# Optimization experiments

Measured on AMD Instinct MI355X. Metric: run time of the kernel, lower is better.

The kernel has to match this reference:

```python
import jax, jax.numpy as jnp
import numpy as np

B, N, D = 8, 4096, 3

def setup_inputs() -> dict:
    key = jax.random.key(0)
    kx, ky = jax.random.split(key)
    x = jax.random.normal(kx, (B, N, D), dtype=jnp.float32)
    y = jax.random.normal(ky, (B, N, D), dtype=jnp.float32)
    return {"x": x, "y": y}

def _nn_diff(A, B_):
    # brute-force NN: squared distances [N, M] via ||a||^2 + ||b||^2 - 2 a.b
    a2 = jnp.sum(A * A, axis=-1)[:, None]
    b2 = jnp.sum(B_ * B_, axis=-1)[None, :]
    d2 = a2 + b2 - 2.0 * (A @ B_.T)
    idx = jnp.argmin(d2, axis=1)            # closest point in B_ for each point in A
    return A - B_[idx]                      # [N, D] signed residuals

def _sigma_pair(S1, S2):
    d12 = _nn_diff(S1, S2)                  # S1 -> S2 residuals
    d21 = _nn_diff(S2, S1)                  # S2 -> S1 residuals
    # torch.std over the whole [N, D] tensor with Bessel's correction (ddof=1)
    std1 = jnp.std(d12, ddof=1)
    std2 = jnp.std(d21, ddof=1)
    return jnp.maximum(std1, std2)

def reference(x, y):
    per_batch = jax.vmap(_sigma_pair)(x, y)  # [B]
    return per_batch.mean()
```

## Files before the change

### kernel.cpp

```cpp
#include <hip/hip_runtime.h>
#include <math.h>

#define NPTS 4096
#define BLK 256
#define NUNITS 16
#define CHUNKS 16
#define CSZ 256
#define TILES 8
#define QGRP 256
#define QGRPS 16
#define GRID1 (NUNITS * QGRPS * CHUNKS)
#define GRID2 (NUNITS * QGRPS)
#define CNT 12288.0f
#define KEY_BYTES ((size_t)NUNITS * CHUNKS * NPTS * 4)

typedef _Float16 half8 __attribute__((ext_vector_type(8)));
typedef float f32x16 __attribute__((ext_vector_type(16)));

__device__ __forceinline__ unsigned umin2(unsigned a, unsigned b) { return a < b ? a : b; }
__device__ __forceinline__ float fmin3(float a, float b, float c) {
  return fminf(fminf(a, b), c);
}

__device__ __forceinline__ float tilemin16(const f32x16 d) {
  const float a0 = fmin3(d[0],  d[1],  d[2]);
  const float a1 = fmin3(d[3],  d[4],  d[5]);
  const float a2 = fmin3(d[6],  d[7],  d[8]);
  const float a3 = fmin3(d[9],  d[10], d[11]);
  const float a4 = fmin3(d[12], d[13], d[14]);
  return fminf(fmin3(a0, a1, a2), fmin3(a3, a4, d[15]));
}

__global__ __launch_bounds__(BLK, 4) void keys_kernel(
    const float* __restrict__ x, const float* __restrict__ y,
    unsigned* __restrict__ keys) {
  __shared__ half8 Ap[2 * CSZ];
  __shared__ half8 Bq[2 * QGRP];

  const int bid   = blockIdx.x;
  const int unit  = bid >> 8;
  const int qg    = (bid >> 4) & 15;
  const int chunk = bid & 15;
  const int b = unit >> 1, dir = unit & 1;
  const float* __restrict__ Q = (dir ? y : x) + (size_t)b * NPTS * 3;
  const float* __restrict__ T = (dir ? x : y) + (size_t)b * NPTS * 3;

  const int tid = threadIdx.x;
  const _Float16 one  = (_Float16)1.0f;
  const _Float16 zero = (_Float16)0.0f;
  const _Float16 n2   = (_Float16)(-2.0f);

  {
    const int tg = chunk * CSZ + tid;
    const float bx = T[3 * tg], by = T[3 * tg + 1], bz = T[3 * tg + 2];
    const float b2 = fmaf(bx, bx, fmaf(by, by, bz * bz));
    const _Float16 bh0 = (_Float16)bx, bh1 = (_Float16)by, bh2 = (_Float16)bz;
    const _Float16 bl0 = (_Float16)(bx - (float)bh0);
    const _Float16 bl1 = (_Float16)(by - (float)bh1);
    const _Float16 bl2 = (_Float16)(bz - (float)bh2);
    const _Float16 s2h = (_Float16)b2;
    const _Float16 s2l = (_Float16)(b2 - (float)s2h);
    half8 lo, hi;
    lo[0] = bh0; lo[1] = bh1; lo[2] = bh2; lo[3] = bl0;
    lo[4] = bl1; lo[5] = bl2; lo[6] = bh0; lo[7] = bh1;
    hi[0] = bh2; hi[1] = s2h; hi[2] = s2l; hi[3] = one;
    hi[4] = one; hi[5] = zero; hi[6] = zero; hi[7] = zero;
    Ap[tid]       = lo;
    Ap[CSZ + tid] = hi;
  }
  {
    const int qq = qg * QGRP + tid;
    const float ax = Q[3 * qq], ay = Q[3 * qq + 1], az = Q[3 * qq + 2];
    const float a2 = fmaf(ax, ax, fmaf(ay, ay, az * az));
    const _Float16 ah0 = (_Float16)ax, ah1 = (_Float16)ay, ah2 = (_Float16)az;
    const _Float16 al0 = (_Float16)(ax - (float)ah0);
    const _Float16 al1 = (_Float16)(ay - (float)ah1);
    const _Float16 al2 = (_Float16)(az - (float)ah2);
    const _Float16 a2h = (_Float16)a2;
    const _Float16 a2l = (_Float16)(a2 - (float)a2h);
    half8 lo, hi;
    lo[0] = n2 * ah0; lo[1] = n2 * ah1; lo[2] = n2 * ah2; lo[3] = n2 * ah0;
    lo[4] = n2 * ah1; lo[5] = n2 * ah2; lo[6] = n2 * al0; lo[7] = n2 * al1;
    hi[0] = n2 * al2; hi[1] = one; hi[2] = one; hi[3] = a2h;
    hi[4] = a2l; hi[5] = zero; hi[6] = zero; hi[7] = zero;
    Bq[tid]        = lo;
    Bq[QGRP + tid] = hi;
  }
  __syncthreads();

  const int lane = tid & 63, w = tid >> 6, ln = lane & 31, hi5 = lane >> 5;
  const half8 bf0 = Bq[hi5 * QGRP + w * 64 + ln];
  const half8 bf1 = Bq[hi5 * QGRP + w * 64 + 32 + ln];

  f32x16 Z;
  #pragma unroll
  for (int r = 0; r < 16; ++r) Z[r] = 0.0f;

  unsigned kacc0 = 0xFFFFFFFFu, kacc1 = 0xFFFFFFFFu;
  const unsigned pbase = (unsigned)(chunk * TILES);

  #pragma unroll
  for (int t = 0; t < TILES; ++t) {
    const half8 af = Ap[hi5 * CSZ + t * 32 + ln];
    const f32x16 d0 = __builtin_amdgcn_mfma_f32_32x32x16_f16(af, bf0, Z, 0, 0, 0);
    const f32x16 d1 = __builtin_amdgcn_mfma_f32_32x32x16_f16(af, bf1, Z, 0, 0, 0);
    const unsigned pay = pbase + (unsigned)t;
    const float m0 = tilemin16(d0);
    const float m1 = tilemin16(d1);
    kacc0 = umin2(kacc0, (__float_as_uint(m0) & 0xFFFFF000u) | pay);
    kacc1 = umin2(kacc1, (__float_as_uint(m1) & 0xFFFFF000u) | pay);
  }

  kacc0 = umin2(kacc0, (unsigned)__shfl_xor((int)kacc0, 32));
  kacc1 = umin2(kacc1, (unsigned)__shfl_xor((int)kacc1, 32));

  if (lane < 32) {
    const unsigned kb = (unsigned)((unit * CHUNKS + chunk) << 12);
    const unsigned q0 = (unsigned)(qg * QGRP + w * 64 + ln);
    keys[kb | q0]        = kacc0;
    keys[kb | (q0 + 32)] = kacc1;
  }
}

__global__ __launch_bounds__(BLK) void resolve_kernel(
    const float* __restrict__ x, const float* __restrict__ y,
    const unsigned* __restrict__ keys, float2* __restrict__ partials) {
  __shared__ float wS[4], wSS[4];

  const int bid  = blockIdx.x;
  const int unit = bid >> 4;
  const int b = unit >> 1, dir = unit & 1;
  const float* __restrict__ Q = (dir ? y : x) + (size_t)b * NPTS * 3;
  const float* __restrict__ T = (dir ? x : y) + (size_t)b * NPTS * 3;
  const int q = ((bid & 15) << 8) + (int)threadIdx.x;

  unsigned bk = 0xFFFFFFFFu;
  #pragma unroll
  for (int c = 0; c < CHUNKS; ++c) {
    bk = umin2(bk, keys[((unsigned)(unit * CHUNKS + c) << 12) | (unsigned)q]);
  }
  const int tbase = (int)(bk & 4095u) * 32;

  const float qx = Q[3 * q], qy = Q[3 * q + 1], qz = Q[3 * q + 2];
  unsigned best = 0xFFFFFFFFu;
  #pragma unroll 8
  for (int i = 0; i < 32; ++i) {
    const int j = tbase + i;
    const float dx = qx - T[3 * j];
    const float dy = qy - T[3 * j + 1];
    const float dz = qz - T[3 * j + 2];
    const float d2 = fmaf(dx, dx, fmaf(dy, dy, dz * dz));
    best = umin2(best, (__float_as_uint(d2) & 0xFFFFFFE0u) | (unsigned)i);
  }
  const int j = tbase + (int)(best & 31u);

  const float rx = qx - T[3 * j];
  const float ry = qy - T[3 * j + 1];
  const float rz = qz - T[3 * j + 2];
  float s  = rx + ry + rz;
  float ss = fmaf(rx, rx, fmaf(ry, ry, rz * rz));

  #pragma unroll
  for (int off = 32; off > 0; off >>= 1) {
    s  += __shfl_down(s, off);
    ss += __shfl_down(ss, off);
  }
  const int wid = threadIdx.x >> 6;
  if ((threadIdx.x & 63) == 0) { wS[wid] = s; wSS[wid] = ss; }
  __syncthreads();
  if (threadIdx.x == 0) {
    partials[bid] = make_float2(wS[0] + wS[1] + wS[2] + wS[3],
                                wSS[0] + wSS[1] + wSS[2] + wSS[3]);
  }
}

__global__ __launch_bounds__(256) void finalize_kernel(
    const float2* __restrict__ partials, float* __restrict__ out) {
  __shared__ float2 sh[GRID2];
  __shared__ float sig[NUNITS];

  sh[threadIdx.x] = partials[threadIdx.x];
  __syncthreads();

  if (threadIdx.x < NUNITS) {
    float S = 0.f, SS = 0.f;
    #pragma unroll
    for (int i = 0; i < QGRPS; ++i) {
      S  += sh[threadIdx.x * QGRPS + i].x;
      SS += sh[threadIdx.x * QGRPS + i].y;
    }
    const float var = (SS - S * S / CNT) / (CNT - 1.0f);
    sig[threadIdx.x] = sqrtf(fmaxf(var, 0.0f));
  }
  __syncthreads();

  if (threadIdx.x == 0) {
    float acc = 0.f;
    #pragma unroll
    for (int b = 0; b < 8; ++b) acc += fmaxf(sig[2 * b], sig[2 * b + 1]);
    out[0] = acc * 0.125f;
  }
}

extern "C" void kernel_launch(void* const* d_in, const int* in_sizes, int n_in,
                              void* d_out, int out_size, void* d_ws, size_t ws_size,
                              hipStream_t stream) {
  const float* x = (const float*)d_in[0];
  const float* y = (const float*)d_in[1];
  float* out = (float*)d_out;

  unsigned* keys   = (unsigned*)d_ws;
  float2*  partials = (float2*)((char*)d_ws + KEY_BYTES);

  hipLaunchKernelGGL(keys_kernel, dim3(GRID1), dim3(BLK), 0, stream, x, y, keys);
  hipLaunchKernelGGL(resolve_kernel, dim3(GRID2), dim3(BLK), 0, stream,
                     x, y, keys, partials);
  hipLaunchKernelGGL(finalize_kernel, dim3(1), dim3(256), 0, stream, partials, out);
}
```

Baseline: 25.62 us.

## Halve key chunks and fuse finalize into resolve via last-block ticket

Doubles the target chunk size per block (CHUNKS 16→8, TILES 8→16), halving the keys-kernel grid and the number of partial keys that resolve must min-reduce. It also folds the finalize kernel into the resolve kernel: each block publishes its partial sums atomically and takes a ticket, and the last block to arrive computes the final sigma mean. This removes one kernel launch and its dependency gap, at the cost of less parallelism in the keys kernel, more LDS per block, and a grid-wide atomic counter that keys_kernel resets.

```diff
diff --git a/kernel.cpp b/kernel.cpp
--- a/kernel.cpp
+++ b/kernel.cpp
@@ -4,9 +4,9 @@
 #define NPTS 4096
 #define BLK 256
 #define NUNITS 16
-#define CHUNKS 16
-#define CSZ 256
-#define TILES 8
+#define CHUNKS 8
+#define CSZ 512
+#define TILES 16
 #define QGRP 256
 #define QGRPS 16
 #define GRID1 (NUNITS * QGRPS * CHUNKS)
@@ -33,25 +33,29 @@
 
 __global__ __launch_bounds__(BLK, 4) void keys_kernel(
     const float* __restrict__ x, const float* __restrict__ y,
-    unsigned* __restrict__ keys) {
+    unsigned* __restrict__ keys, unsigned* __restrict__ ticket) {
   __shared__ half8 Ap[2 * CSZ];
   __shared__ half8 Bq[2 * QGRP];
 
   const int bid   = blockIdx.x;
-  const int unit  = bid >> 8;
-  const int qg    = (bid >> 4) & 15;
-  const int chunk = bid & 15;
+  const int unit  = bid >> 7;
+  const int qg    = (bid >> 3) & 15;
+  const int chunk = bid & 7;
   const int b = unit >> 1, dir = unit & 1;
   const float* __restrict__ Q = (dir ? y : x) + (size_t)b * NPTS * 3;
   const float* __restrict__ T = (dir ? x : y) + (size_t)b * NPTS * 3;
 
   const int tid = threadIdx.x;
+  if (bid == 0 && tid == 0) *ticket = 0;
+
   const _Float16 one  = (_Float16)1.0f;
   const _Float16 zero = (_Float16)0.0f;
   const _Float16 n2   = (_Float16)(-2.0f);
 
-  {
-    const int tg = chunk * CSZ + tid;
+  #pragma unroll
+  for (int k = 0; k < 2; ++k) {
+    const int i  = tid + k * BLK;
+    const int tg = chunk * CSZ + i;
     const float bx = T[3 * tg], by = T[3 * tg + 1], bz = T[3 * tg + 2];
     const float b2 = fmaf(bx, bx, fmaf(by, by, bz * bz));
     const _Float16 bh0 = (_Float16)bx, bh1 = (_Float16)by, bh2 = (_Float16)bz;
@@ -65,8 +69,8 @@
     lo[4] = bl1; lo[5] = bl2; lo[6] = bh0; lo[7] = bh1;
     hi[0] = bh2; hi[1] = s2h; hi[2] = s2l; hi[3] = one;
     hi[4] = one; hi[5] = zero; hi[6] = zero; hi[7] = zero;
-    Ap[tid]       = lo;
-    Ap[CSZ + tid] = hi;
+    Ap[i]       = lo;
+    Ap[CSZ + i] = hi;
   }
   {
     const int qq = qg * QGRP + tid;
@@ -122,17 +126,23 @@
   }
 }
 
-__global__ __launch_bounds__(BLK) void resolve_kernel(
+__global__ __launch_bounds__(BLK) void resolve_finalize_kernel(
     const float* __restrict__ x, const float* __restrict__ y,
-    const unsigned* __restrict__ keys, float2* __restrict__ partials) {
+    const unsigned* __restrict__ keys,
+    unsigned long long* __restrict__ partials,
+    unsigned* __restrict__ ticket, float* __restrict__ out) {
   __shared__ float wS[4], wSS[4];
+  __shared__ unsigned lastsh;
+  __shared__ float2 sh[GRID2];
+  __shared__ float sig[NUNITS];
 
   const int bid  = blockIdx.x;
   const int unit = bid >> 4;
   const int b = unit >> 1, dir = unit & 1;
   const float* __restrict__ Q = (dir ? y : x) + (size_t)b * NPTS * 3;
   const float* __restrict__ T = (dir ? x : y) + (size_t)b * NPTS * 3;
-  const int q = ((bid & 15) << 8) + (int)threadIdx.x;
+  const int tid = threadIdx.x;
+  const int q = ((bid & 15) << 8) + tid;
 
   unsigned bk = 0xFFFFFFFFu;
   #pragma unroll
@@ -165,39 +175,46 @@
     s  += __shfl_down(s, off);
     ss += __shfl_down(ss, off);
   }
-  const int wid = threadIdx.x >> 6;
-  if ((threadIdx.x & 63) == 0) { wS[wid] = s; wSS[wid] = ss; }
-  __syncthreads();
-  if (threadIdx.x == 0) {
-    partials[bid] = make_float2(wS[0] + wS[1] + wS[2] + wS[3],
-                                wSS[0] + wSS[1] + wSS[2] + wSS[3]);
-  }
-}
-
-__global__ __launch_bounds__(256) void finalize_kernel(
-    const float2* __restrict__ partials, float* __restrict__ out) {
-  __shared__ float2 sh[GRID2];
-  __shared__ float sig[NUNITS];
-
-  sh[threadIdx.x] = partials[threadIdx.x];
-  __syncthreads();
-
-  if (threadIdx.x < NUNITS) {
+  const int wid = tid >> 6;
+  if ((tid & 63) == 0) { wS[wid] = s; wSS[wid] = ss; }
+  __syncthreads();
+
+  if (tid == 0) {
+    const float S  = wS[0]  + wS[1]  + wS[2]  + wS[3];
+    const float SS = wSS[0] + wSS[1] + wSS[2] + wSS[3];
+    const unsigned long long pv =
+        ((unsigned long long)__float_as_uint(SS) << 32) | __float_as_uint(S);
+    atomicExch(&partials[bid], pv);
+    __threadfence();
+    lastsh = atomicAdd(ticket, 1u);
+  }
+  __syncthreads();
+  if (lastsh != GRID2 - 1) return;
+
+  __threadfence();
+  {
+    const unsigned long long pv = atomicAdd(&partials[tid], 0ULL);
+    sh[tid] = make_float2(__uint_as_float((unsigned)(pv & 0xFFFFFFFFull)),
+                          __uint_as_float((unsigned)(pv >> 32)));
+  }
+  __syncthreads();
+
+  if (tid < NUNITS) {
     float S = 0.f, SS = 0.f;
     #pragma unroll
     for (int i = 0; i < QGRPS; ++i) {
-      S  += sh[threadIdx.x * QGRPS + i].x;
-      SS += sh[threadIdx.x * QGRPS + i].y;
+      S  += sh[tid * QGRPS + i].x;
+      SS += sh[tid * QGRPS + i].y;
     }
     const float var = (SS - S * S / CNT) / (CNT - 1.0f);
-    sig[threadIdx.x] = sqrtf(fmaxf(var, 0.0f));
-  }
-  __syncthreads();
-
-  if (threadIdx.x == 0) {
+    sig[tid] = sqrtf(fmaxf(var, 0.0f));
+  }
+  __syncthreads();
+
+  if (tid == 0) {
     float acc = 0.f;
     #pragma unroll
-    for (int b = 0; b < 8; ++b) acc += fmaxf(sig[2 * b], sig[2 * b + 1]);
+    for (int b2 = 0; b2 < 8; ++b2) acc += fmaxf(sig[2 * b2], sig[2 * b2 + 1]);
     out[0] = acc * 0.125f;
   }
 }
@@ -209,11 +226,14 @@
   const float* y = (const float*)d_in[1];
   float* out = (float*)d_out;
 
-  unsigned* keys   = (unsigned*)d_ws;
-  float2*  partials = (float2*)((char*)d_ws + KEY_BYTES);
-
-  hipLaunchKernelGGL(keys_kernel, dim3(GRID1), dim3(BLK), 0, stream, x, y, keys);
-  hipLaunchKernelGGL(resolve_kernel, dim3(GRID2), dim3(BLK), 0, stream,
-                     x, y, keys, partials);
-  hipLaunchKernelGGL(finalize_kernel, dim3(1), dim3(256), 0, stream, partials, out);
-}
+  unsigned* keys = (unsigned*)d_ws;
+  unsigned long long* partials =
+      (unsigned long long*)((char*)d_ws + KEY_BYTES);
+  unsigned* ticket =
+      (unsigned*)((char*)d_ws + KEY_BYTES + GRID2 * sizeof(unsigned long long));
+
+  hipLaunchKernelGGL(keys_kernel, dim3(GRID1), dim3(BLK), 0, stream,
+                     x, y, keys, ticket);
+  hipLaunchKernelGGL(resolve_finalize_kernel, dim3(GRID2), dim3(BLK), 0, stream,
+                     x, y, keys, partials, ticket, out);
+}
```

Result: slower. 27.89 us (+8.8%).

## Fuse key scan and resolve into one full-scan kernel per query group

Applied to the files above, without the earlier changes.

The separate keys and resolve kernels are replaced by a single kernel. Each block stages all 4096 target points into LDS in two 2048-point phases, runs the MFMA distance scan for 128 queries, then refines the winning 32-point tile and reduces the residual sums in place. This removes the global key workspace write and re-read and one kernel launch. In exchange, each target point is converted to fp16 hi/lo form twice as often in total, each block uses much more LDS, and the grid shrinks to 512 blocks with lower occupancy. Half of each wave sits idle during the refinement step.

```diff
diff --git a/kernel.cpp b/kernel.cpp
--- a/kernel.cpp
+++ b/kernel.cpp
@@ -4,15 +4,11 @@
 #define NPTS 4096
 #define BLK 256
 #define NUNITS 16
-#define CHUNKS 16
-#define CSZ 256
-#define TILES 8
-#define QGRP 256
-#define QGRPS 16
-#define GRID1 (NUNITS * QGRPS * CHUNKS)
-#define GRID2 (NUNITS * QGRPS)
+#define QGRP 128
+#define QGRPS 32
+#define GRID1 (NUNITS * QGRPS)
+#define PHT 2048
 #define CNT 12288.0f
-#define KEY_BYTES ((size_t)NUNITS * CHUNKS * NPTS * 4)
 
 typedef _Float16 half8 __attribute__((ext_vector_type(8)));
 typedef float f32x16 __attribute__((ext_vector_type(16)));
@@ -31,16 +27,15 @@
   return fminf(fmin3(a0, a1, a2), fmin3(a3, a4, d[15]));
 }
 
-__global__ __launch_bounds__(BLK, 4) void keys_kernel(
+__global__ __launch_bounds__(BLK, 2) void fullscan_kernel(
     const float* __restrict__ x, const float* __restrict__ y,
-    unsigned* __restrict__ keys) {
-  __shared__ half8 Ap[2 * CSZ];
+    float2* __restrict__ partials) {
+  __shared__ half8 Ap[2 * PHT];
   __shared__ half8 Bq[2 * QGRP];
+  __shared__ float wS[4], wSS[4];
 
-  const int bid   = blockIdx.x;
-  const int unit  = bid >> 8;
-  const int qg    = (bid >> 4) & 15;
-  const int chunk = bid & 15;
+  const int bid  = blockIdx.x;
+  const int unit = bid >> 5, qg = bid & 31;
   const int b = unit >> 1, dir = unit & 1;
   const float* __restrict__ Q = (dir ? y : x) + (size_t)b * NPTS * 3;
   const float* __restrict__ T = (dir ? x : y) + (size_t)b * NPTS * 3;
@@ -50,25 +45,7 @@
   const _Float16 zero = (_Float16)0.0f;
   const _Float16 n2   = (_Float16)(-2.0f);
 
-  {
-    const int tg = chunk * CSZ + tid;
-    const float bx = T[3 * tg], by = T[3 * tg + 1], bz = T[3 * tg + 2];
-    const float b2 = fmaf(bx, bx, fmaf(by, by, bz * bz));
-    const _Float16 bh0 = (_Float16)bx, bh1 = (_Float16)by, bh2 = (_Float16)bz;
-    const _Float16 bl0 = (_Float16)(bx - (float)bh0);
-    const _Float16 bl1 = (_Float16)(by - (float)bh1);
-    const _Float16 bl2 = (_Float16)(bz - (float)bh2);
-    const _Float16 s2h = (_Float16)b2;
-    const _Float16 s2l = (_Float16)(b2 - (float)s2h);
-    half8 lo, hi;
-    lo[0] = bh0; lo[1] = bh1; lo[2] = bh2; lo[3] = bl0;
-    lo[4] = bl1; lo[5] = bl2; lo[6] = bh0; lo[7] = bh1;
-    hi[0] = bh2; hi[1] = s2h; hi[2] = s2l; hi[3] = one;
-    hi[4] = one; hi[5] = zero; hi[6] = zero; hi[7] = zero;
-    Ap[tid]       = lo;
-    Ap[CSZ + tid] = hi;
-  }
-  {
+  if (tid < QGRP) {
     const int qq = qg * QGRP + tid;
     const float ax = Q[3 * qq], ay = Q[3 * qq + 1], az = Q[3 * qq + 2];
     const float a2 = fmaf(ax, ax, fmaf(ay, ay, az * az));
@@ -86,100 +63,95 @@
     Bq[tid]        = lo;
     Bq[QGRP + tid] = hi;
   }
-  __syncthreads();
 
   const int lane = tid & 63, w = tid >> 6, ln = lane & 31, hi5 = lane >> 5;
-  const half8 bf0 = Bq[hi5 * QGRP + w * 64 + ln];
-  const half8 bf1 = Bq[hi5 * QGRP + w * 64 + 32 + ln];
-
+  unsigned kacc0 = 0xFFFFFFFFu, kacc1 = 0xFFFFFFFFu;
   f32x16 Z;
   #pragma unroll
   for (int r = 0; r < 16; ++r) Z[r] = 0.0f;
 
-  unsigned kacc0 = 0xFFFFFFFFu, kacc1 = 0xFFFFFFFFu;
-  const unsigned pbase = (unsigned)(chunk * TILES);
+  half8 bf;
+  for (int c = 0; c < 2; ++c) {
+    __syncthreads();
+    #pragma unroll
+    for (int k = 0; k < 8; ++k) {
+      const int i  = tid + k * BLK;
+      const int tg = c * PHT + i;
+      const float bx = T[3 * tg], by = T[3 * tg + 1], bz = T[3 * tg + 2];
+      const float b2 = fmaf(bx, bx, fmaf(by, by, bz * bz));
+      const _Float16 bh0 = (_Float16)bx, bh1 = (_Float16)by, bh2 = (_Float16)bz;
+      const _Float16 bl0 = (_Float16)(bx - (float)bh0);
+      const _Float16 bl1 = (_Float16)(by - (float)bh1);
+      const _Float16 bl2 = (_Float16)(bz - (float)bh2);
+      const _Float16 s2h = (_Float16)b2;
+      const _Float16 s2l = (_Float16)(b2 - (float)s2h);
+      half8 lo, hi;
+      lo[0] = bh0; lo[1] = bh1; lo[2] = bh2; lo[3] = bl0;
+      lo[4] = bl1; lo[5] = bl2; lo[6] = bh0; lo[7] = bh1;
+      hi[0] = bh2; hi[1] = s2h; hi[2] = s2l; hi[3] = one;
+      hi[4] = one; hi[5] = zero; hi[6] = zero; hi[7] = zero;
+      Ap[i]       = lo;
+      Ap[PHT + i] = hi;
+    }
+    __syncthreads();
+    if (c == 0) bf = Bq[hi5 * QGRP + w * 32 + ln];
 
-  #pragma unroll
-  for (int t = 0; t < TILES; ++t) {
-    const half8 af = Ap[hi5 * CSZ + t * 32 + ln];
-    const f32x16 d0 = __builtin_amdgcn_mfma_f32_32x32x16_f16(af, bf0, Z, 0, 0, 0);
-    const f32x16 d1 = __builtin_amdgcn_mfma_f32_32x32x16_f16(af, bf1, Z, 0, 0, 0);
-    const unsigned pay = pbase + (unsigned)t;
-    const float m0 = tilemin16(d0);
-    const float m1 = tilemin16(d1);
-    kacc0 = umin2(kacc0, (__float_as_uint(m0) & 0xFFFFF000u) | pay);
-    kacc1 = umin2(kacc1, (__float_as_uint(m1) & 0xFFFFF000u) | pay);
+    const unsigned cb = (unsigned)(c * (PHT / 32));
+    #pragma unroll 4
+    for (int t = 0; t < PHT / 32; ++t) {
+      const half8 af = Ap[hi5 * PHT + t * 32 + ln];
+      const f32x16 d = __builtin_amdgcn_mfma_f32_32x32x16_f16(af, bf, Z, 0, 0, 0);
+      const unsigned key = (__float_as_uint(tilemin16(d)) & 0xFFFFF000u) | (cb + (unsigned)t);
+      if (t & 1) kacc1 = umin2(kacc1, key);
+      else       kacc0 = umin2(kacc0, key);
+    }
   }
+  unsigned kacc = umin2(kacc0, kacc1);
+  kacc = umin2(kacc, (unsigned)__shfl_xor((int)kacc, 32));
 
-  kacc0 = umin2(kacc0, (unsigned)__shfl_xor((int)kacc0, 32));
-  kacc1 = umin2(kacc1, (unsigned)__shfl_xor((int)kacc1, 32));
-
+  float s = 0.f, ss = 0.f;
   if (lane < 32) {
-    const unsigned kb = (unsigned)((unit * CHUNKS + chunk) << 12);
-    const unsigned q0 = (unsigned)(qg * QGRP + w * 64 + ln);
-    keys[kb | q0]        = kacc0;
-    keys[kb | (q0 + 32)] = kacc1;
+    const int q = qg * QGRP + w * 32 + ln;
+    const int tbase = (int)(kacc & 4095u) * 32;
+    const float qx = Q[3 * q], qy = Q[3 * q + 1], qz = Q[3 * q + 2];
+    unsigned best = 0xFFFFFFFFu;
+    #pragma unroll 8
+    for (int i = 0; i < 32; ++i) {
+      const int j = tbase + i;
+      const float dx = qx - T[3 * j];
+      const float dy = qy - T[3 * j + 1];
+      const float dz = qz - T[3 * j + 2];
+      const float d2 = fmaf(dx, dx, fmaf(dy, dy, dz * dz));
+      best = umin2(best, (__float_as_uint(d2) & 0xFFFFFFE0u) | (unsigned)i);
+    }
+    const int j = tbase + (int)(best & 31u);
+    const float rx = qx - T[3 * j];
+    const float ry = qy - T[3 * j + 1];
+    const float rz = qz - T[3 * j + 2];
+    s  = rx + ry + rz;
+    ss = fmaf(rx, rx, fmaf(ry, ry, rz * rz));
   }
-}
-
-__global__ __launch_bounds__(BLK) void resolve_kernel(
-    const float* __restrict__ x, const float* __restrict__ y,
-    const unsigned* __restrict__ keys, float2* __restrict__ partials) {
-  __shared__ float wS[4], wSS[4];
-
-  const int bid  = blockIdx.x;
-  const int unit = bid >> 4;
-  const int b = unit >> 1, dir = unit & 1;
-  const float* __restrict__ Q = (dir ? y : x) + (size_t)b * NPTS * 3;
-  const float* __restrict__ T = (dir ? x : y) + (size_t)b * NPTS * 3;
-  const int q = ((bid & 15) << 8) + (int)threadIdx.x;
-
-  unsigned bk = 0xFFFFFFFFu;
-  #pragma unroll
-  for (int c = 0; c < CHUNKS; ++c) {
-    bk = umin2(bk, keys[((unsigned)(unit * CHUNKS + c) << 12) | (unsigned)q]);
-  }
-  const int tbase = (int)(bk & 4095u) * 32;
-
-  const float qx = Q[3 * q], qy = Q[3 * q + 1], qz = Q[3 * q + 2];
-  unsigned best = 0xFFFFFFFFu;
-  #pragma unroll 8
-  for (int i = 0; i < 32; ++i) {
-    const int j = tbase + i;
-    const float dx = qx - T[3 * j];
-    const float dy = qy - T[3 * j + 1];
-    const float dz = qz - T[3 * j + 2];
-    const float d2 = fmaf(dx, dx, fmaf(dy, dy, dz * dz));
-    best = umin2(best, (__float_as_uint(d2) & 0xFFFFFFE0u) | (unsigned)i);
-  }
-  const int j = tbase + (int)(best & 31u);
-
-  const float rx = qx - T[3 * j];
-  const float ry = qy - T[3 * j + 1];
-  const float rz = qz - T[3 * j + 2];
-  float s  = rx + ry + rz;
-  float ss = fmaf(rx, rx, fmaf(ry, ry, rz * rz));
 
   #pragma unroll
   for (int off = 32; off > 0; off >>= 1) {
     s  += __shfl_down(s, off);
     ss += __shfl_down(ss, off);
   }
-  const int wid = threadIdx.x >> 6;
-  if ((threadIdx.x & 63) == 0) { wS[wid] = s; wSS[wid] = ss; }
+  if ((tid & 63) == 0) { wS[w] = s; wSS[w] = ss; }
   __syncthreads();
-  if (threadIdx.x == 0) {
+  if (tid == 0) {
     partials[bid] = make_float2(wS[0] + wS[1] + wS[2] + wS[3],
                                 wSS[0] + wSS[1] + wSS[2] + wSS[3]);
   }
 }
 
-__global__ __launch_bounds__(256) void finalize_kernel(
+__global__ __launch_bounds__(BLK) void finalize_kernel(
     const float2* __restrict__ partials, float* __restrict__ out) {
-  __shared__ float2 sh[GRID2];
+  __shared__ float2 sh[GRID1];
   __shared__ float sig[NUNITS];
 
-  sh[threadIdx.x] = partials[threadIdx.x];
+  sh[threadIdx.x]       = partials[threadIdx.x];
+  sh[threadIdx.x + BLK] = partials[threadIdx.x + BLK];
   __syncthreads();
 
   if (threadIdx.x < NUNITS) {
@@ -208,12 +180,10 @@
   const float* x = (const float*)d_in[0];
   const float* y = (const float*)d_in[1];
   float* out = (float*)d_out;
+  float2* partials = (float2*)d_ws;
 
-  unsigned* keys   = (unsigned*)d_ws;
-  float2*  partials = (float2*)((char*)d_ws + KEY_BYTES);
-
-  hipLaunchKernelGGL(keys_kernel, dim3(GRID1), dim3(BLK), 0, stream, x, y, keys);
-  hipLaunchKernelGGL(resolve_kernel, dim3(GRID2), dim3(BLK), 0, stream,
-                     x, y, keys, partials);
-  hipLaunchKernelGGL(finalize_kernel, dim3(1), dim3(256), 0, stream, partials, out);
+  hipLaunchKernelGGL(fullscan_kernel, dim3(GRID1), dim3(BLK), 0, stream,
+                     x, y, partials);
+  hipLaunchKernelGGL(finalize_kernel, dim3(1), dim3(BLK), 0, stream,
+                     partials, out);
 }
```

New measurement: 23.30 us (median of 2 runs). 1.1x faster.
